# Kernel optimization log

Hardware: AMD Instinct MI355X
Metric: run time of the kernel (lower is better)

The kernel has to match this reference:

```python
import jax, jax.numpy as jnp
import numpy as np

BS, NPTS, NM, D = 8, 8192, 32, 512  # objects, points/object, masks/object, feature dim


def setup_inputs() -> dict:
    key = jax.random.key(0)
    k1, k2, k3 = jax.random.split(key, 3)
    net_out = jax.random.normal(k1, (BS * NPTS, D), dtype=jnp.float32)
    mask_embs = jax.random.normal(k2, (BS * NM, D), dtype=jnp.float32)
    mask_pts = (jax.random.uniform(k3, (BS, NM, NPTS)) < 0.5).astype(jnp.float32)
    pt_offset = (jnp.arange(1, BS + 1) * NPTS).astype(jnp.int32)  # per-object end idx
    logit_scale = jnp.float32(2.6593)  # ln(1/0.07), CLIP-style
    return {
        "net_out": net_out,
        "mask_embs": mask_embs,
        "mask_pts": mask_pts,
        "logit_scale": logit_scale,
        "pt_offset": pt_offset,
    }


def reference(net_out, mask_embs, mask_pts, logit_scale, pt_offset):
    bs, nm, npts = mask_pts.shape
    d = net_out.shape[1]
    n_total = bs * nm

    # ragged per-object mask_pt @ net_out[start:end] -> uniform batched matmul
    net = net_out.reshape(bs, npts, d)
    sum_feats = jnp.einsum('bmp,bpd->bmd', mask_pts, net).reshape(n_total, d)

    mask_npts = jnp.sum(mask_pts, axis=-1).reshape(n_total, 1)  # points per mask
    nopts = (mask_npts[:, 0] == 0)                              # empty masks -> ignored
    avg_feats = sum_feats / (mask_npts + 1e-12)

    logits = (mask_embs @ avg_feats.T) * jnp.exp(logit_scale)   # [N, N]

    idx = jnp.arange(n_total)
    valid = ~nopts  # target == -100 (ignore) for empty masks, else arange diagonal
    texts_loss = jnp.where(valid, -jax.nn.log_softmax(logits, axis=-1)[idx, idx], 0.0)
    pts_loss = jnp.where(valid, -jax.nn.log_softmax(logits.T, axis=-1)[idx, idx], 0.0)

    def nonzero_avg(l):
        cnt = jnp.sum(l > 0)
        return jnp.where(cnt > 0, jnp.sum(l) / jnp.maximum(cnt, 1), 0.0)

    return (nonzero_avg(texts_loss) + nonzero_avg(pts_loss)) / 2.0
```

## Files before the change

kernel.cpp:

```cpp
#include <hip/hip_runtime.h>
#include <hip/hip_bf16.h>
#include <math.h>

#define BS 8
#define NPTS 8192
#define NM 32
#define D 512
#define NT (BS*NM)
#define KC 16
#define KCHUNK (NPTS/KC)
#define TILES (KCHUNK/32)
#define DC 8
#define DCHUNK (D/DC)
#define NWORDS (NPTS/32)

#define LOG2E 1.44269504088896f
#define LN2   0.69314718055995f

typedef short short8 __attribute__((ext_vector_type(8)));
typedef float f32x4 __attribute__((ext_vector_type(4)));

static constexpr size_t OFF_SUMF = 0;
static constexpr size_t OFF_CNTS = OFF_SUMF + (size_t)NT*D;
static constexpr size_t OFF_BITS = OFF_CNTS + NT;
static constexpr size_t OFF_LOG  = OFF_BITS + (size_t)NT*NWORDS;
static constexpr size_t OFF_RLSE = OFF_LOG + (size_t)NT*NT;
static constexpr size_t OFF_CLSE = OFF_RLSE + NT;
static constexpr size_t OFF_TICK = OFF_CLSE + NT;

__device__ __forceinline__ short bf16_rne(float f) {
  return __builtin_bit_cast(short, __float2bfloat16(f));
}

__global__ __launch_bounds__(256) void kp_prep(const float* __restrict__ mpts,
                                               unsigned int* __restrict__ mbits,
                                               float* __restrict__ cnts,
                                               float* __restrict__ sumf,
                                               int* __restrict__ ticket) {
  const int n = blockIdx.x;
  const int t = threadIdx.x;
  if (n == 0 && t == 0) *ticket = 0;
  const float4* mp = (const float4*)(mpts + ((size_t)n << 13) + t * 32);
  unsigned int u = 0;
  #pragma unroll
  for (int q = 0; q < 8; ++q) {
    const float4 v = mp[q];
    u |= (v.x != 0.f ? 1u : 0u) << (q * 4 + 0);
    u |= (v.y != 0.f ? 1u : 0u) << (q * 4 + 1);
    u |= (v.z != 0.f ? 1u : 0u) << (q * 4 + 2);
    u |= (v.w != 0.f ? 1u : 0u) << (q * 4 + 3);
  }
  mbits[n * NWORDS + t] = u;
  ((float2*)(sumf + ((size_t)n << 9)))[t] = make_float2(0.f, 0.f);
  int c = __popc(u);
  #pragma unroll
  for (int o = 32; o > 0; o >>= 1) c += __shfl_down(c, o, 64);
  __shared__ int red[4];
  if ((t & 63) == 0) red[t >> 6] = c;
  __syncthreads();
  if (t == 0) cnts[n] = (float)(red[0] + red[1] + red[2] + red[3]);
}

__global__ __launch_bounds__(256, 8) void k1_mfma(const float* __restrict__ net,
                                                  const unsigned int* __restrict__ mbits,
                                                  float* __restrict__ sumf) {
  const int bx = blockIdx.x;
  const int dc = bx & 7;
  const int kc = (bx >> 3) & 15;
  const int b  = bx >> 7;
  const int w    = threadIdx.x >> 6;
  const int lane = threadIdx.x & 63;
  const int lhi = lane >> 4, llo = lane & 15;
  const int k0 = kc * KCHUNK;
  const int d0 = dc * DCHUNK + w * 16;

  const unsigned int* r0 = mbits + (size_t)(b * NM + llo) * NWORDS + kc * TILES;
  const unsigned int* r1 = r0 + (size_t)16 * NWORDS;

  const float* np_ = net + (((size_t)(b * NPTS + k0 + lhi * 8)) << 9) + d0 + llo;

  f32x4 acc0 = {0.f, 0.f, 0.f, 0.f};
  f32x4 acc1 = {0.f, 0.f, 0.f, 0.f};
  const int sh = lhi * 8;

  #pragma unroll 4
  for (int t = 0; t < TILES; ++t) {
    const unsigned int u0 = r0[t];
    const unsigned int u1 = r1[t];

    float bv[8];
    #pragma unroll
    for (int j = 0; j < 8; ++j) bv[j] = np_[(size_t)j << 9];

    short8 bf, a0f, a1f;
    #pragma unroll
    for (int j = 0; j < 8; ++j) bf[j] = bf16_rne(bv[j]);
    const unsigned int b0 = (u0 >> sh) & 0xffu;
    const unsigned int b1 = (u1 >> sh) & 0xffu;
    #pragma unroll
    for (int j = 0; j < 8; ++j) {
      a0f[j] = (short)(-(int)((b0 >> j) & 1u) & 0x3F80);
      a1f[j] = (short)(-(int)((b1 >> j) & 1u) & 0x3F80);
    }

    acc0 = __builtin_amdgcn_mfma_f32_16x16x32_bf16(a0f, bf, acc0, 0, 0, 0);
    acc1 = __builtin_amdgcn_mfma_f32_16x16x32_bf16(a1f, bf, acc1, 0, 0, 0);

    np_ += (size_t)32 << 9;
  }

  float* sp = sumf + (((size_t)(b * NM)) << 9) + d0 + llo;
  #pragma unroll
  for (int j = 0; j < 4; ++j) {
    atomicAdd(sp + ((size_t)(lhi * 4 + j) << 9),      acc0[j]);
    atomicAdd(sp + ((size_t)(16 + lhi * 4 + j) << 9), acc1[j]);
  }
}

__global__ __launch_bounds__(128) void k2_logits(const float* __restrict__ embs,
                                                 const float* __restrict__ sumf,
                                                 const float* __restrict__ cnts,
                                                 const float* __restrict__ lsc,
                                                 float* __restrict__ logits) {
  const int h = threadIdx.x >> 6;
  const int lane = threadIdx.x & 63;
  const int wt = blockIdx.x;
  const int ti = wt >> 4, tj = wt & 15;
  const int lhi = lane >> 4, llo = lane & 15;

  const float* ea = embs + (((size_t)(ti * 16 + llo)) << 9) + h * 256 + lhi * 8;
  const float* sv = sumf + (((size_t)(tj * 16 + llo)) << 9) + h * 256 + lhi * 8;
  f32x4 acc = {0.f, 0.f, 0.f, 0.f};
  #pragma unroll
  for (int kk = 0; kk < 8; ++kk) {
    const float4 e0 = *(const float4*)(ea);
    const float4 e1 = *(const float4*)(ea + 4);
    const float4 v0 = *(const float4*)(sv);
    const float4 v1 = *(const float4*)(sv + 4);
    const float ev[8] = {e0.x, e0.y, e0.z, e0.w, e1.x, e1.y, e1.z, e1.w};
    const float vv[8] = {v0.x, v0.y, v0.z, v0.w, v1.x, v1.y, v1.z, v1.w};
    short8 ef, vf;
    #pragma unroll
    for (int j = 0; j < 8; ++j) { ef[j] = bf16_rne(ev[j]); vf[j] = bf16_rne(vv[j]); }
    acc = __builtin_amdgcn_mfma_f32_16x16x32_bf16(ef, vf, acc, 0, 0, 0);
    ea += 32; sv += 32;
  }

  __shared__ float part[64 * 4];
  if (h == 1) *(float4*)(&part[lane * 4]) = make_float4(acc[0], acc[1], acc[2], acc[3]);
  __syncthreads();
  if (h == 0) {
    const float4 p = *(const float4*)(&part[lane * 4]);
    const float scale = expf(lsc[0]);
    const float invc = scale / (cnts[tj * 16 + llo] + 1e-12f);
    float* lp = logits + (size_t)(ti * 16) * NT + tj * 16 + llo;
    lp[(size_t)(lhi * 4 + 0) * NT] = (acc[0] + p.x) * invc;
    lp[(size_t)(lhi * 4 + 1) * NT] = (acc[1] + p.y) * invc;
    lp[(size_t)(lhi * 4 + 2) * NT] = (acc[2] + p.z) * invc;
    lp[(size_t)(lhi * 4 + 3) * NT] = (acc[3] + p.w) * invc;
  }
}

__global__ __launch_bounds__(256) void k3_lse(const float* __restrict__ logits,
                                              float* __restrict__ rowlse,
                                              float* __restrict__ clse,
                                              const float* __restrict__ cnts,
                                              int* __restrict__ ticket,
                                              float* __restrict__ out) {
  const int g = blockIdx.x;
  const int r = threadIdx.x >> 4;
  const int c = threadIdx.x & 15;
  __shared__ float red[16][17];
  if (g < 16) {
    const int col = g * 16 + c;
    float mx = -1e30f;
    #pragma unroll 4
    for (int kk = 0; kk < 16; ++kk)
      mx = fmaxf(mx, logits[(size_t)(kk * 16 + r) * NT + col]);
    red[r][c] = mx; __syncthreads();
    for (int st = 8; st; st >>= 1) { if (r < st) red[r][c] = fmaxf(red[r][c], red[r + st][c]); __syncthreads(); }
    const float mx2 = red[0][c] * LOG2E; __syncthreads();
    float s = 0.f;
    #pragma unroll 4
    for (int kk = 0; kk < 16; ++kk)
      s += exp2f(logits[(size_t)(kk * 16 + r) * NT + col] * LOG2E - mx2);
    red[r][c] = s; __syncthreads();
    for (int st = 8; st; st >>= 1) { if (r < st) red[r][c] += red[r + st][c]; __syncthreads(); }
    if (r == 0) clse[col] = (mx2 + log2f(red[0][c])) * LN2;
  } else {
    const int row = (g - 16) * 16 + r;
    float mx = -1e30f;
    #pragma unroll 4
    for (int kk = 0; kk < 16; ++kk)
      mx = fmaxf(mx, logits[(size_t)row * NT + kk * 16 + c]);
    #pragma unroll
    for (int o = 8; o; o >>= 1) mx = fmaxf(mx, __shfl_xor(mx, o, 64));
    const float mx2 = mx * LOG2E;
    float s = 0.f;
    #pragma unroll 4
    for (int kk = 0; kk < 16; ++kk)
      s += exp2f(logits[(size_t)row * NT + kk * 16 + c] * LOG2E - mx2);
    #pragma unroll
    for (int o = 8; o; o >>= 1) s += __shfl_xor(s, o, 64);
    if (c == 0) rowlse[row] = (mx2 + log2f(s)) * LN2;
  }

  __shared__ int slast;
  __syncthreads();
  if (threadIdx.x == 0) {
    __threadfence();
    slast = (atomicAdd(ticket, 1) == 31);
  }
  __syncthreads();
  if (!slast) return;
  __threadfence();

  const int i = threadIdx.x;
  const float diag = logits[(size_t)i * NT + i];
  const bool valid = cnts[i] > 0.f;
  const float tl = valid ? (rowlse[i] - diag) : 0.f;
  const float pl = valid ? (clse[i] - diag) : 0.f;

  __shared__ float fred[4][256];
  fred[0][i] = tl;
  fred[1][i] = (tl > 0.f) ? 1.f : 0.f;
  fred[2][i] = pl;
  fred[3][i] = (pl > 0.f) ? 1.f : 0.f;
  __syncthreads();
  for (int st = 128; st > 0; st >>= 1) {
    if (i < st) {
      fred[0][i] += fred[0][i + st];
      fred[1][i] += fred[1][i + st];
      fred[2][i] += fred[2][i + st];
      fred[3][i] += fred[3][i + st];
    }
    __syncthreads();
  }
  if (i == 0) {
    const float a1 = (fred[1][0] > 0.f) ? fred[0][0] / fmaxf(fred[1][0], 1.f) : 0.f;
    const float a2 = (fred[3][0] > 0.f) ? fred[2][0] / fmaxf(fred[3][0], 1.f) : 0.f;
    out[0] = 0.5f * (a1 + a2);
  }
}

extern "C" void kernel_launch(void* const* d_in, const int* in_sizes, int n_in,
                              void* d_out, int out_size, void* d_ws, size_t ws_size,
                              hipStream_t stream) {
  const float* net  = (const float*)d_in[0];
  const float* embs = (const float*)d_in[1];
  const float* mpts = (const float*)d_in[2];
  const float* lsc  = (const float*)d_in[3];

  float* ws     = (float*)d_ws;
  float* sumf   = ws + OFF_SUMF;
  float* cnts   = ws + OFF_CNTS;
  unsigned int* mbits = (unsigned int*)(ws + OFF_BITS);
  float* logits = ws + OFF_LOG;
  float* rowlse = ws + OFF_RLSE;
  float* clse   = ws + OFF_CLSE;
  int*   ticket = (int*)(ws + OFF_TICK);
  float* outp   = (float*)d_out;

  kp_prep<<<dim3(NT), dim3(256), 0, stream>>>(mpts, mbits, cnts, sumf, ticket);
  k1_mfma<<<dim3(BS * KC * DC), dim3(256), 0, stream>>>(net, mbits, sumf);
  k2_logits<<<dim3(NT), dim3(128), 0, stream>>>(embs, sumf, cnts, lsc, logits);
  k3_lse<<<dim3(32), dim3(256), 0, stream>>>(logits, rowlse, clse, cnts, ticket, outp);
}
```

Baseline: 48.85 us.

## Fuse logits and LSE kernels via grid barrier; ballot-based mask packing

Merges the logits kernel and the log-sum-exp/loss kernel into one launch. The first 32 blocks spin on an atomic counter until all 256 logits blocks have written their tiles. The logits K-reduction is split over four waves instead of two. The prep kernel now packs mask bits with wave ballots and coalesced scalar loads instead of per-thread float4 loops. This removes one kernel launch and gap. In exchange it depends on all 256 blocks being co-resident or otherwise scheduled, so the spin-wait cannot deadlock.

```diff
diff --git a/kernel.cpp b/kernel.cpp
--- a/kernel.cpp
+++ b/kernel.cpp
@@ -36,29 +36,28 @@
                                                unsigned int* __restrict__ mbits,
                                                float* __restrict__ cnts,
                                                float* __restrict__ sumf,
-                                               int* __restrict__ ticket) {
+                                               int* __restrict__ tickets) {
   const int n = blockIdx.x;
   const int t = threadIdx.x;
-  if (n == 0 && t == 0) *ticket = 0;
-  const float4* mp = (const float4*)(mpts + ((size_t)n << 13) + t * 32);
-  unsigned int u = 0;
-  #pragma unroll
-  for (int q = 0; q < 8; ++q) {
-    const float4 v = mp[q];
-    u |= (v.x != 0.f ? 1u : 0u) << (q * 4 + 0);
-    u |= (v.y != 0.f ? 1u : 0u) << (q * 4 + 1);
-    u |= (v.z != 0.f ? 1u : 0u) << (q * 4 + 2);
-    u |= (v.w != 0.f ? 1u : 0u) << (q * 4 + 3);
-  }
-  mbits[n * NWORDS + t] = u;
+  const int w = t >> 6, lane = t & 63;
+  if (n == 0 && t < 2) tickets[t] = 0;
+
+  const float* base = mpts + ((size_t)n << 13) + w * 2048;
+  uint2* wout = (uint2*)(mbits + (size_t)n * NWORDS + w * 64);
+  int cnt = 0;
+  #pragma unroll 8
+  for (int i = 0; i < 32; ++i) {
+    const float v = base[i * 64 + lane];
+    const unsigned long long m = __ballot(v != 0.f);
+    cnt += __popcll(m);
+    if (lane == 0) wout[i] = make_uint2((unsigned)m, (unsigned)(m >> 32));
+  }
+  __shared__ float redc[4];
+  if (lane == 0) redc[w] = (float)cnt;
+  __syncthreads();
+  if (t == 0) cnts[n] = redc[0] + redc[1] + redc[2] + redc[3];
+
   ((float2*)(sumf + ((size_t)n << 9)))[t] = make_float2(0.f, 0.f);
-  int c = __popc(u);
-  #pragma unroll
-  for (int o = 32; o > 0; o >>= 1) c += __shfl_down(c, o, 64);
-  __shared__ int red[4];
-  if ((t & 63) == 0) red[t >> 6] = c;
-  __syncthreads();
-  if (t == 0) cnts[n] = (float)(red[0] + red[1] + red[2] + red[3]);
 }
 
 __global__ __launch_bounds__(256, 8) void k1_mfma(const float* __restrict__ net,
@@ -117,56 +116,69 @@
   }
 }
 
-__global__ __launch_bounds__(128) void k2_logits(const float* __restrict__ embs,
+__global__ __launch_bounds__(256) void k23_fused(const float* __restrict__ embs,
                                                  const float* __restrict__ sumf,
                                                  const float* __restrict__ cnts,
                                                  const float* __restrict__ lsc,
-                                                 float* __restrict__ logits) {
+                                                 float* __restrict__ logits,
+                                                 float* __restrict__ rowlse,
+                                                 float* __restrict__ clse,
+                                                 int* __restrict__ tickets,
+                                                 float* __restrict__ out) {
   const int h = threadIdx.x >> 6;
   const int lane = threadIdx.x & 63;
   const int wt = blockIdx.x;
   const int ti = wt >> 4, tj = wt & 15;
   const int lhi = lane >> 4, llo = lane & 15;
 
-  const float* ea = embs + (((size_t)(ti * 16 + llo)) << 9) + h * 256 + lhi * 8;
-  const float* sv = sumf + (((size_t)(tj * 16 + llo)) << 9) + h * 256 + lhi * 8;
-  f32x4 acc = {0.f, 0.f, 0.f, 0.f};
-  #pragma unroll
-  for (int kk = 0; kk < 8; ++kk) {
-    const float4 e0 = *(const float4*)(ea);
-    const float4 e1 = *(const float4*)(ea + 4);
-    const float4 v0 = *(const float4*)(sv);
-    const float4 v1 = *(const float4*)(sv + 4);
-    const float ev[8] = {e0.x, e0.y, e0.z, e0.w, e1.x, e1.y, e1.z, e1.w};
-    const float vv[8] = {v0.x, v0.y, v0.z, v0.w, v1.x, v1.y, v1.z, v1.w};
-    short8 ef, vf;
-    #pragma unroll
-    for (int j = 0; j < 8; ++j) { ef[j] = bf16_rne(ev[j]); vf[j] = bf16_rne(vv[j]); }
-    acc = __builtin_amdgcn_mfma_f32_16x16x32_bf16(ef, vf, acc, 0, 0, 0);
-    ea += 32; sv += 32;
-  }
-
-  __shared__ float part[64 * 4];
-  if (h == 1) *(float4*)(&part[lane * 4]) = make_float4(acc[0], acc[1], acc[2], acc[3]);
-  __syncthreads();
-  if (h == 0) {
-    const float4 p = *(const float4*)(&part[lane * 4]);
-    const float scale = expf(lsc[0]);
-    const float invc = scale / (cnts[tj * 16 + llo] + 1e-12f);
-    float* lp = logits + (size_t)(ti * 16) * NT + tj * 16 + llo;
-    lp[(size_t)(lhi * 4 + 0) * NT] = (acc[0] + p.x) * invc;
-    lp[(size_t)(lhi * 4 + 1) * NT] = (acc[1] + p.y) * invc;
-    lp[(size_t)(lhi * 4 + 2) * NT] = (acc[2] + p.z) * invc;
-    lp[(size_t)(lhi * 4 + 3) * NT] = (acc[3] + p.w) * invc;
-  }
-}
-
-__global__ __launch_bounds__(256) void k3_lse(const float* __restrict__ logits,
-                                              float* __restrict__ rowlse,
-                                              float* __restrict__ clse,
-                                              const float* __restrict__ cnts,
-                                              int* __restrict__ ticket,
-                                              float* __restrict__ out) {
+  {
+    const float* ea = embs + (((size_t)(ti * 16 + llo)) << 9) + h * 128 + lhi * 8;
+    const float* sv = sumf + (((size_t)(tj * 16 + llo)) << 9) + h * 128 + lhi * 8;
+    f32x4 acc = {0.f, 0.f, 0.f, 0.f};
+    #pragma unroll
+    for (int kk = 0; kk < 4; ++kk) {
+      const float4 e0 = *(const float4*)(ea);
+      const float4 e1 = *(const float4*)(ea + 4);
+      const float4 v0 = *(const float4*)(sv);
+      const float4 v1 = *(const float4*)(sv + 4);
+      const float ev[8] = {e0.x, e0.y, e0.z, e0.w, e1.x, e1.y, e1.z, e1.w};
+      const float vv[8] = {v0.x, v0.y, v0.z, v0.w, v1.x, v1.y, v1.z, v1.w};
+      short8 ef, vf;
+      #pragma unroll
+      for (int j = 0; j < 8; ++j) { ef[j] = bf16_rne(ev[j]); vf[j] = bf16_rne(vv[j]); }
+      acc = __builtin_amdgcn_mfma_f32_16x16x32_bf16(ef, vf, acc, 0, 0, 0);
+      ea += 32; sv += 32;
+    }
+
+    __shared__ float part[4][64][4];
+    *(float4*)(&part[h][lane][0]) = make_float4(acc[0], acc[1], acc[2], acc[3]);
+    __syncthreads();
+    if (h == 0) {
+      const float4 p1 = *(const float4*)(&part[1][lane][0]);
+      const float4 p2 = *(const float4*)(&part[2][lane][0]);
+      const float4 p3 = *(const float4*)(&part[3][lane][0]);
+      const float scale = expf(lsc[0]);
+      const float invc = scale / (cnts[tj * 16 + llo] + 1e-12f);
+      float* lp = logits + (size_t)(ti * 16) * NT + tj * 16 + llo;
+      lp[(size_t)(lhi * 4 + 0) * NT] = (acc[0] + p1.x + p2.x + p3.x) * invc;
+      lp[(size_t)(lhi * 4 + 1) * NT] = (acc[1] + p1.y + p2.y + p3.y) * invc;
+      lp[(size_t)(lhi * 4 + 2) * NT] = (acc[2] + p1.z + p2.z + p3.z) * invc;
+      lp[(size_t)(lhi * 4 + 3) * NT] = (acc[3] + p1.w + p2.w + p3.w) * invc;
+    }
+  }
+
+  __threadfence();
+  __syncthreads();
+  if (threadIdx.x == 0) atomicAdd(&tickets[0], 1);
+  if (blockIdx.x >= 32) return;
+  if (threadIdx.x == 0) {
+    while (__hip_atomic_load(&tickets[0], __ATOMIC_ACQUIRE,
+                             __HIP_MEMORY_SCOPE_AGENT) < 256)
+      __builtin_amdgcn_s_sleep(2);
+  }
+  __syncthreads();
+  __threadfence();
+
   const int g = blockIdx.x;
   const int r = threadIdx.x >> 4;
   const int c = threadIdx.x & 15;
@@ -209,7 +221,7 @@
   __syncthreads();
   if (threadIdx.x == 0) {
     __threadfence();
-    slast = (atomicAdd(ticket, 1) == 31);
+    slast = (atomicAdd(&tickets[1], 1) == 31);
   }
   __syncthreads();
   if (!slast) return;
@@ -258,11 +270,11 @@
   float* logits = ws + OFF_LOG;
   float* rowlse = ws + OFF_RLSE;
   float* clse   = ws + OFF_CLSE;
-  int*   ticket = (int*)(ws + OFF_TICK);
+  int*   tickets = (int*)(ws + OFF_TICK);
   float* outp   = (float*)d_out;
 
-  kp_prep<<<dim3(NT), dim3(256), 0, stream>>>(mpts, mbits, cnts, sumf, ticket);
+  kp_prep<<<dim3(NT), dim3(256), 0, stream>>>(mpts, mbits, cnts, sumf, tickets);
   k1_mfma<<<dim3(BS * KC * DC), dim3(256), 0, stream>>>(net, mbits, sumf);
-  k2_logits<<<dim3(NT), dim3(128), 0, stream>>>(embs, sumf, cnts, lsc, logits);
-  k3_lse<<<dim3(32), dim3(256), 0, stream>>>(logits, rowlse, clse, cnts, ticket, outp);
-}
+  k23_fused<<<dim3(NT), dim3(256), 0, stream>>>(embs, sumf, cnts, lsc, logits,
+                                                rowlse, clse, tickets, outp);
+}
```

After: 75.32 us. +54.2%, slower.
